# Optimization experiments

Measured on AMD Instinct MI355X. Metric: run time of the kernel, lower is better.

## Reference

```python
import jax, jax.numpy as jnp
import numpy as np

FIELD_DIMS = [1000000, 100000, 1008, 1004, 102, 1000, 500, 50, 112, 107]
B = 16384
EMB = 32
DENSE = 16
MLP = [256, 128, 64]
BN_EPS = 1e-5
V_TOTAL = int(np.sum(FIELD_DIMS))
OFFSETS = jnp.asarray(np.concatenate([[0], np.cumsum(FIELD_DIMS)[:-1]]), dtype=jnp.int64)


def _xavier(key, fan_out, fan_in):
    lim = float(np.sqrt(6.0 / (fan_in + fan_out)))
    return jax.random.uniform(key, (fan_out, fan_in), jnp.float32, -lim, lim)


def setup_inputs() -> dict:
    key = jax.random.key(0)
    ks = jax.random.split(key, 16)
    # per-field in-range indices, stacked to [B, n_fields]
    sparse_cols = [jax.random.randint(jax.random.fold_in(ks[0], i), (B,), 0, d)
                   for i, d in enumerate(FIELD_DIMS)]
    sparse_inputs = jnp.stack(sparse_cols, axis=1).astype(jnp.int64)
    dense_inputs = jax.random.normal(ks[1], (B, DENSE), jnp.float32)
    # concatenated embedding / first-order bias tables (same math as per-field nn.Embedding)
    emb_table = 0.01 * jax.random.normal(ks[2], (V_TOTAL, EMB), jnp.float32)
    bias_table = 0.01 * jax.random.normal(ks[3], (V_TOTAL, 1), jnp.float32)
    fm_bias = jnp.zeros((1,), jnp.float32)
    dims = [len(FIELD_DIMS) * EMB + DENSE] + MLP
    params = {}
    for li in range(len(MLP)):
        params[f"W{li}"] = _xavier(ks[4 + li], dims[li + 1], dims[li])
        params[f"b{li}"] = jnp.zeros((dims[li + 1],), jnp.float32)
        params[f"g{li}"] = jnp.ones((dims[li + 1],), jnp.float32)
        params[f"be{li}"] = jnp.zeros((dims[li + 1],), jnp.float32)
    Wo = _xavier(ks[10], 1, MLP[-1])
    bo = jnp.zeros((1,), jnp.float32)
    return dict(sparse_inputs=sparse_inputs, dense_inputs=dense_inputs,
                emb_table=emb_table, bias_table=bias_table, fm_bias=fm_bias,
                Wo=Wo, bo=bo, **params)


def reference(sparse_inputs, dense_inputs, emb_table, bias_table, fm_bias,
              Wo, bo, W0, b0, g0, be0, W1, b1, g1, be1, W2, b2, g2, be2):
    idx = sparse_inputs + OFFSETS[None, :]           # [B, F] global rows
    field_embs = emb_table[idx]                      # [B, F, E] multi-table gather
    # FM first order: sum of per-field scalar biases
    fm_first = bias_table[idx][..., 0].sum(axis=1)   # [B]
    # FM second order: 0.5 * sum_d ((sum_f e)^2 - sum_f e^2)
    s = field_embs.sum(axis=1)                       # [B, E]
    sq = (field_embs * field_embs).sum(axis=1)       # [B, E]
    fm_second = 0.5 * (s * s - sq).sum(axis=-1)      # [B]
    fm_out = fm_bias[0] + fm_first + fm_second
    # deep component (BatchNorm in eval mode at init stats: mean=0, var=1; dropout=identity)
    x = jnp.concatenate([field_embs.reshape(field_embs.shape[0], -1), dense_inputs], axis=-1)
    inv = 1.0 / jnp.sqrt(1.0 + BN_EPS)
    for W, b, g, be in ((W0, b0, g0, be0), (W1, b1, g1, be1), (W2, b2, g2, be2)):
        h = x @ W.T + b
        h = h * (g * inv) + be
        x = jax.nn.relu(h)
    deep_out = (x @ Wo.T + bo)[:, 0]
    return jax.nn.sigmoid(fm_out + deep_out)
```

## Files before the change

kernel.cpp:

```cpp
#include <hip/hip_runtime.h>
#include <hip/hip_bf16.h>
#include <math.h>

#define BROWS 16384
#define NF    10
#define EMB   32
#define DENSE 16
#define K0S   352
#define K0    336
#define N0    256
#define N1    128
#define N2    64
#define BN_INV 0.99999500003749969f

__constant__ int c_offsets[NF] = {
    0, 1000000, 1100000, 1101008, 1102012,
    1102114, 1103114, 1103614, 1103664, 1103776
};

typedef short  bf16x8 __attribute__((ext_vector_type(8)));
typedef float  f32x4  __attribute__((ext_vector_type(4)));

static __device__ __forceinline__ unsigned short f2bf(float x) {
    union { float f; unsigned u; } c; c.f = x;
    unsigned r = (c.u + 0x7FFFu + ((c.u >> 16) & 1u)) >> 16;
    return (unsigned short)r;
}

__global__ __launch_bounds__(256) void k_wconv_all(
    const float* __restrict__ W0, const float* __restrict__ W1,
    const float* __restrict__ W2,
    unsigned short* __restrict__ W0b, unsigned short* __restrict__ W1b,
    unsigned short* __restrict__ W2b)
{
    int i = blockIdx.x * 256 + threadIdx.x;
    if (i < N0 * K0S) {
        int r = i / K0S, c = i - r * K0S;
        W0b[i] = f2bf(c < K0 ? W0[r * K0 + c] : 0.f);
    } else if (i < N0 * K0S + N1 * N0) {
        int j = i - N0 * K0S;
        W1b[j] = f2bf(W1[j]);
    } else {
        int j = i - (N0 * K0S + N1 * N0);
        W2b[j] = f2bf(W2[j]);
    }
}

__global__ __launch_bounds__(256) void k_fused_l0(
    const int*   __restrict__ sparse,
    const float* __restrict__ dense,
    const float* __restrict__ emb,
    const float* __restrict__ bias_tab,
    const float* __restrict__ fm_bias,
    const unsigned short* __restrict__ W0b,
    const float* __restrict__ b0, const float* __restrict__ g0,
    const float* __restrict__ be0,
    unsigned short* __restrict__ x1,
    float* __restrict__ fm)
{
    const int tid  = threadIdx.x;
    const int wave = tid >> 6;
    const int lane = tid & 63;
    const int l16  = lane & 15;
    const int quad = lane >> 4;
    const int arow = blockIdx.x * 64 + wave * 16 + l16;

    int idx[NF];
#pragma unroll
    for (int f = 0; f < NF; ++f)
        idx[f] = sparse[arow * NF + f] + c_offsets[f];

    float first = 0.f;
    if (quad == 0) {
#pragma unroll
        for (int f = 0; f < NF; ++f) first += bias_tab[idx[f]];
    }

    float s8[8];
#pragma unroll
    for (int j = 0; j < 8; ++j) s8[j] = 0.f;
    float sq = 0.f;

    f32x4 acc[16];
#pragma unroll
    for (int nt = 0; nt < 16; ++nt) acc[nt] = (f32x4){0.f, 0.f, 0.f, 0.f};

#pragma unroll
    for (int f = 0; f < NF; ++f) {
        const float4* ep = (const float4*)(emb + (size_t)idx[f] * EMB + quad * 8);
        float4 v0 = ep[0];
        float4 v1 = ep[1];
        s8[0] += v0.x; s8[1] += v0.y; s8[2] += v0.z; s8[3] += v0.w;
        s8[4] += v1.x; s8[5] += v1.y; s8[6] += v1.z; s8[7] += v1.w;
        sq += v0.x*v0.x + v0.y*v0.y + v0.z*v0.z + v0.w*v0.w
            + v1.x*v1.x + v1.y*v1.y + v1.z*v1.z + v1.w*v1.w;
        bf16x8 a;
        a[0] = (short)f2bf(v0.x); a[1] = (short)f2bf(v0.y);
        a[2] = (short)f2bf(v0.z); a[3] = (short)f2bf(v0.w);
        a[4] = (short)f2bf(v1.x); a[5] = (short)f2bf(v1.y);
        a[6] = (short)f2bf(v1.z); a[7] = (short)f2bf(v1.w);
        const unsigned short* wp = W0b + (size_t)l16 * K0S + f * 32 + quad * 8;
#pragma unroll
        for (int nt = 0; nt < 16; ++nt) {
            bf16x8 w = *(const bf16x8*)(wp + (size_t)(nt * 16) * K0S);
            acc[nt] = __builtin_amdgcn_mfma_f32_16x16x32_bf16(a, w, acc[nt], 0, 0, 0);
        }
    }

    {
        bf16x8 a;
        if (quad < 2) {
            const float4* dp = (const float4*)(dense + arow * DENSE + quad * 8);
            float4 v0 = dp[0];
            float4 v1 = dp[1];
            a[0] = (short)f2bf(v0.x); a[1] = (short)f2bf(v0.y);
            a[2] = (short)f2bf(v0.z); a[3] = (short)f2bf(v0.w);
            a[4] = (short)f2bf(v1.x); a[5] = (short)f2bf(v1.y);
            a[6] = (short)f2bf(v1.z); a[7] = (short)f2bf(v1.w);
        } else {
#pragma unroll
            for (int j = 0; j < 8; ++j) a[j] = 0;
        }
        const unsigned short* wp = W0b + (size_t)l16 * K0S + 320 + quad * 8;
#pragma unroll
        for (int nt = 0; nt < 16; ++nt) {
            bf16x8 w = *(const bf16x8*)(wp + (size_t)(nt * 16) * K0S);
            acc[nt] = __builtin_amdgcn_mfma_f32_16x16x32_bf16(a, w, acc[nt], 0, 0, 0);
        }
    }

    float ss = 0.f;
#pragma unroll
    for (int j = 0; j < 8; ++j) ss += s8[j] * s8[j];
    ss += __shfl_xor(ss, 16); ss += __shfl_xor(ss, 32);
    sq += __shfl_xor(sq, 16); sq += __shfl_xor(sq, 32);
    first += __shfl_xor(first, 16); first += __shfl_xor(first, 32);
    if (quad == 0)
        fm[arow] = fm_bias[0] + first + 0.5f * (ss - sq);

#pragma unroll
    for (int nt = 0; nt < 16; ++nt) {
        int col = nt * 16 + l16;
        float sc = g0[col] * BN_INV;
        float tb = fmaf(b0[col], sc, be0[col]);
#pragma unroll
        for (int r = 0; r < 4; ++r) {
            int orow = blockIdx.x * 64 + wave * 16 + quad * 4 + r;
            float v = fmaf(acc[nt][r], sc, tb);
            v = v > 0.f ? v : 0.f;
            x1[(size_t)orow * N0 + col] = f2bf(v);
        }
    }
}

__global__ __launch_bounds__(256) void k_fused_tail(
    const unsigned short* __restrict__ x1,
    const unsigned short* __restrict__ W1b,
    const float* __restrict__ b1, const float* __restrict__ g1,
    const float* __restrict__ be1,
    const unsigned short* __restrict__ W2b,
    const float* __restrict__ b2, const float* __restrict__ g2,
    const float* __restrict__ be2,
    const float* __restrict__ Wo,
    const float* __restrict__ bo,
    const float* __restrict__ fm,
    float* __restrict__ out)
{
    __shared__ unsigned short h2[64][N1 + 8];

    const int tid  = threadIdx.x;
    const int wave = tid >> 6;
    const int lane = tid & 63;
    const int l16  = lane & 15;
    const int quad = lane >> 4;
    const int bm   = blockIdx.x * 64;
    const int arow = bm + wave * 16 + l16;

    f32x4 acc1[8];
#pragma unroll
    for (int nt = 0; nt < 8; ++nt) acc1[nt] = (f32x4){0.f, 0.f, 0.f, 0.f};
    const unsigned short* ap1 = x1 + (size_t)arow * N0 + quad * 8;
#pragma unroll
    for (int ks = 0; ks < 8; ++ks) {
        bf16x8 a = *(const bf16x8*)(ap1 + ks * 32);
        const unsigned short* wp = W1b + (size_t)l16 * N0 + ks * 32 + quad * 8;
#pragma unroll
        for (int nt = 0; nt < 8; ++nt) {
            bf16x8 w = *(const bf16x8*)(wp + (size_t)(nt * 16) * N0);
            acc1[nt] = __builtin_amdgcn_mfma_f32_16x16x32_bf16(a, w, acc1[nt], 0, 0, 0);
        }
    }
#pragma unroll
    for (int nt = 0; nt < 8; ++nt) {
        int col = nt * 16 + l16;
        float sc = g1[col] * BN_INV;
        float tb = fmaf(b1[col], sc, be1[col]);
#pragma unroll
        for (int r = 0; r < 4; ++r) {
            float v = fmaf(acc1[nt][r], sc, tb);
            v = v > 0.f ? v : 0.f;
            h2[wave * 16 + quad * 4 + r][col] = f2bf(v);
        }
    }
    __syncthreads();

    f32x4 acc2[4];
#pragma unroll
    for (int nt = 0; nt < 4; ++nt) acc2[nt] = (f32x4){0.f, 0.f, 0.f, 0.f};
#pragma unroll
    for (int ks = 0; ks < 4; ++ks) {
        bf16x8 a = *(const bf16x8*)(&h2[wave * 16 + l16][ks * 32 + quad * 8]);
        const unsigned short* wp = W2b + (size_t)l16 * N1 + ks * 32 + quad * 8;
#pragma unroll
        for (int nt = 0; nt < 4; ++nt) {
            bf16x8 w = *(const bf16x8*)(wp + (size_t)(nt * 16) * N1);
            acc2[nt] = __builtin_amdgcn_mfma_f32_16x16x32_bf16(a, w, acc2[nt], 0, 0, 0);
        }
    }

    float p[4] = {0.f, 0.f, 0.f, 0.f};
#pragma unroll
    for (int nt = 0; nt < 4; ++nt) {
        int col = nt * 16 + l16;
        float sc = g2[col] * BN_INV;
        float tb = fmaf(b2[col], sc, be2[col]);
        float wo = Wo[col];
#pragma unroll
        for (int r = 0; r < 4; ++r) {
            float v = fmaf(acc2[nt][r], sc, tb);
            v = v > 0.f ? v : 0.f;
            p[r] = fmaf(v, wo, p[r]);
        }
    }
#pragma unroll
    for (int r = 0; r < 4; ++r) {
        p[r] += __shfl_xor(p[r], 1);
        p[r] += __shfl_xor(p[r], 2);
        p[r] += __shfl_xor(p[r], 4);
        p[r] += __shfl_xor(p[r], 8);
    }
    if (l16 == 0) {
#pragma unroll
        for (int r = 0; r < 4; ++r) {
            int orow = bm + wave * 16 + quad * 4 + r;
            float z = fm[orow] + p[r] + bo[0];
            out[orow] = 1.f / (1.f + expf(-z));
        }
    }
}

extern "C" void kernel_launch(void* const* d_in, const int* in_sizes, int n_in,
                              void* d_out, int out_size, void* d_ws, size_t ws_size,
                              hipStream_t stream)
{
    const int*   sparse   = (const int*)  d_in[0];
    const float* dense    = (const float*)d_in[1];
    const float* emb      = (const float*)d_in[2];
    const float* bias_tab = (const float*)d_in[3];
    const float* fm_bias  = (const float*)d_in[4];
    const float* Wo       = (const float*)d_in[5];
    const float* bo       = (const float*)d_in[6];
    const float* W0 = (const float*)d_in[7];
    const float* b0 = (const float*)d_in[8];
    const float* g0 = (const float*)d_in[9];
    const float* be0= (const float*)d_in[10];
    const float* W1 = (const float*)d_in[11];
    const float* b1 = (const float*)d_in[12];
    const float* g1 = (const float*)d_in[13];
    const float* be1= (const float*)d_in[14];
    const float* W2 = (const float*)d_in[15];
    const float* b2 = (const float*)d_in[16];
    const float* g2 = (const float*)d_in[17];
    const float* be2= (const float*)d_in[18];

    float* out = (float*)d_out;

    char* p = (char*)d_ws;
    unsigned short* x1  = (unsigned short*)p; p += (size_t)BROWS * N0 * 2;
    unsigned short* W0b = (unsigned short*)p; p += (size_t)N0 * K0S * 2;
    unsigned short* W1b = (unsigned short*)p; p += (size_t)N1 * N0 * 2;
    unsigned short* W2b = (unsigned short*)p; p += (size_t)N2 * N1 * 2;
    float*          fm  = (float*)p;

    k_wconv_all<<<(N0 * K0S + N1 * N0 + N2 * N1) / 256, 256, 0, stream>>>(
        W0, W1, W2, W0b, W1b, W2b);

    k_fused_l0<<<BROWS / 64, 256, 0, stream>>>(
        sparse, dense, emb, bias_tab, fm_bias, W0b, b0, g0, be0, x1, fm);

    k_fused_tail<<<BROWS / 64, 256, 0, stream>>>(
        x1, W1b, b1, g1, be1, W2b, b2, g2, be2, Wo, bo, fm, out);
}
```

Before: 245.9 us.

## Fuse embedding layer and MLP tail into one kernel with LDS intermediates

```diff
diff --git a/kernel.cpp b/kernel.cpp
--- a/kernel.cpp
+++ b/kernel.cpp
@@ -46,7 +46,7 @@
     }
 }
 
-__global__ __launch_bounds__(256) void k_fused_l0(
+__global__ __launch_bounds__(256) void k_fused_all(
     const int*   __restrict__ sparse,
     const float* __restrict__ dense,
     const float* __restrict__ emb,
@@ -55,106 +55,6 @@
     const unsigned short* __restrict__ W0b,
     const float* __restrict__ b0, const float* __restrict__ g0,
     const float* __restrict__ be0,
-    unsigned short* __restrict__ x1,
-    float* __restrict__ fm)
-{
-    const int tid  = threadIdx.x;
-    const int wave = tid >> 6;
-    const int lane = tid & 63;
-    const int l16  = lane & 15;
-    const int quad = lane >> 4;
-    const int arow = blockIdx.x * 64 + wave * 16 + l16;
-
-    int idx[NF];
-#pragma unroll
-    for (int f = 0; f < NF; ++f)
-        idx[f] = sparse[arow * NF + f] + c_offsets[f];
-
-    float first = 0.f;
-    if (quad == 0) {
-#pragma unroll
-        for (int f = 0; f < NF; ++f) first += bias_tab[idx[f]];
-    }
-
-    float s8[8];
-#pragma unroll
-    for (int j = 0; j < 8; ++j) s8[j] = 0.f;
-    float sq = 0.f;
-
-    f32x4 acc[16];
-#pragma unroll
-    for (int nt = 0; nt < 16; ++nt) acc[nt] = (f32x4){0.f, 0.f, 0.f, 0.f};
-
-#pragma unroll
-    for (int f = 0; f < NF; ++f) {
-        const float4* ep = (const float4*)(emb + (size_t)idx[f] * EMB + quad * 8);
-        float4 v0 = ep[0];
-        float4 v1 = ep[1];
-        s8[0] += v0.x; s8[1] += v0.y; s8[2] += v0.z; s8[3] += v0.w;
-        s8[4] += v1.x; s8[5] += v1.y; s8[6] += v1.z; s8[7] += v1.w;
-        sq += v0.x*v0.x + v0.y*v0.y + v0.z*v0.z + v0.w*v0.w
-            + v1.x*v1.x + v1.y*v1.y + v1.z*v1.z + v1.w*v1.w;
-        bf16x8 a;
-        a[0] = (short)f2bf(v0.x); a[1] = (short)f2bf(v0.y);
-        a[2] = (short)f2bf(v0.z); a[3] = (short)f2bf(v0.w);
-        a[4] = (short)f2bf(v1.x); a[5] = (short)f2bf(v1.y);
-        a[6] = (short)f2bf(v1.z); a[7] = (short)f2bf(v1.w);
-        const unsigned short* wp = W0b + (size_t)l16 * K0S + f * 32 + quad * 8;
-#pragma unroll
-        for (int nt = 0; nt < 16; ++nt) {
-            bf16x8 w = *(const bf16x8*)(wp + (size_t)(nt * 16) * K0S);
-            acc[nt] = __builtin_amdgcn_mfma_f32_16x16x32_bf16(a, w, acc[nt], 0, 0, 0);
-        }
-    }
-
-    {
-        bf16x8 a;
-        if (quad < 2) {
-            const float4* dp = (const float4*)(dense + arow * DENSE + quad * 8);
-            float4 v0 = dp[0];
-            float4 v1 = dp[1];
-            a[0] = (short)f2bf(v0.x); a[1] = (short)f2bf(v0.y);
-            a[2] = (short)f2bf(v0.z); a[3] = (short)f2bf(v0.w);
-            a[4] = (short)f2bf(v1.x); a[5] = (short)f2bf(v1.y);
-            a[6] = (short)f2bf(v1.z); a[7] = (short)f2bf(v1.w);
-        } else {
-#pragma unroll
-            for (int j = 0; j < 8; ++j) a[j] = 0;
-        }
-        const unsigned short* wp = W0b + (size_t)l16 * K0S + 320 + quad * 8;
-#pragma unroll
-        for (int nt = 0; nt < 16; ++nt) {
-            bf16x8 w = *(const bf16x8*)(wp + (size_t)(nt * 16) * K0S);
-            acc[nt] = __builtin_amdgcn_mfma_f32_16x16x32_bf16(a, w, acc[nt], 0, 0, 0);
-        }
-    }
-
-    float ss = 0.f;
-#pragma unroll
-    for (int j = 0; j < 8; ++j) ss += s8[j] * s8[j];
-    ss += __shfl_xor(ss, 16); ss += __shfl_xor(ss, 32);
-    sq += __shfl_xor(sq, 16); sq += __shfl_xor(sq, 32);
-    first += __shfl_xor(first, 16); first += __shfl_xor(first, 32);
-    if (quad == 0)
-        fm[arow] = fm_bias[0] + first + 0.5f * (ss - sq);
-
-#pragma unroll
-    for (int nt = 0; nt < 16; ++nt) {
-        int col = nt * 16 + l16;
-        float sc = g0[col] * BN_INV;
-        float tb = fmaf(b0[col], sc, be0[col]);
-#pragma unroll
-        for (int r = 0; r < 4; ++r) {
-            int orow = blockIdx.x * 64 + wave * 16 + quad * 4 + r;
-            float v = fmaf(acc[nt][r], sc, tb);
-            v = v > 0.f ? v : 0.f;
-            x1[(size_t)orow * N0 + col] = f2bf(v);
-        }
-    }
-}
-
-__global__ __launch_bounds__(256) void k_fused_tail(
-    const unsigned short* __restrict__ x1,
     const unsigned short* __restrict__ W1b,
     const float* __restrict__ b1, const float* __restrict__ g1,
     const float* __restrict__ be1,
@@ -163,43 +63,108 @@
     const float* __restrict__ be2,
     const float* __restrict__ Wo,
     const float* __restrict__ bo,
-    const float* __restrict__ fm,
     float* __restrict__ out)
 {
-    __shared__ unsigned short h2[64][N1 + 8];
+    __shared__ unsigned short x1s[32][N0 + 2];
+    __shared__ unsigned short h2s[32][N1 + 2];
+    __shared__ float fmld[32];
+    __shared__ float partial[2][32];
 
     const int tid  = threadIdx.x;
     const int wave = tid >> 6;
     const int lane = tid & 63;
     const int l16  = lane & 15;
     const int quad = lane >> 4;
-    const int bm   = blockIdx.x * 64;
-    const int arow = bm + wave * 16 + l16;
+    const int rg   = wave & 1;
+    const int hh   = wave >> 1;
+    const int bm   = blockIdx.x * 32;
+    const int arow = bm + rg * 16 + l16;
+
+    int idx[NF];
+#pragma unroll
+    for (int f = 0; f < NF; ++f)
+        idx[f] = sparse[arow * NF + f] + c_offsets[f];
+
+    float first = 0.f, sq = 0.f;
+    float s8[8];
+#pragma unroll
+    for (int j = 0; j < 8; ++j) s8[j] = 0.f;
+
+    if (hh == 0 && quad == 0) {
+#pragma unroll
+        for (int f = 0; f < NF; ++f) first += bias_tab[idx[f]];
+    }
 
     f32x4 acc1[8];
 #pragma unroll
     for (int nt = 0; nt < 8; ++nt) acc1[nt] = (f32x4){0.f, 0.f, 0.f, 0.f};
-    const unsigned short* ap1 = x1 + (size_t)arow * N0 + quad * 8;
-#pragma unroll
-    for (int ks = 0; ks < 8; ++ks) {
-        bf16x8 a = *(const bf16x8*)(ap1 + ks * 32);
-        const unsigned short* wp = W1b + (size_t)l16 * N0 + ks * 32 + quad * 8;
+
+    const unsigned short* wp0 = W0b + (size_t)(hh * 128 + l16) * K0S + quad * 8;
+
+#pragma unroll
+    for (int f = 0; f < NF; ++f) {
+        const float4* ep = (const float4*)(emb + (size_t)idx[f] * EMB) + quad * 2;
+        float4 v0 = ep[0];
+        float4 v1 = ep[1];
+        if (hh == 0) {
+            s8[0] += v0.x; s8[1] += v0.y; s8[2] += v0.z; s8[3] += v0.w;
+            s8[4] += v1.x; s8[5] += v1.y; s8[6] += v1.z; s8[7] += v1.w;
+            sq += v0.x*v0.x + v0.y*v0.y + v0.z*v0.z + v0.w*v0.w
+                + v1.x*v1.x + v1.y*v1.y + v1.z*v1.z + v1.w*v1.w;
+        }
+        bf16x8 a;
+        a[0] = (short)f2bf(v0.x); a[1] = (short)f2bf(v0.y);
+        a[2] = (short)f2bf(v0.z); a[3] = (short)f2bf(v0.w);
+        a[4] = (short)f2bf(v1.x); a[5] = (short)f2bf(v1.y);
+        a[6] = (short)f2bf(v1.z); a[7] = (short)f2bf(v1.w);
 #pragma unroll
         for (int nt = 0; nt < 8; ++nt) {
-            bf16x8 w = *(const bf16x8*)(wp + (size_t)(nt * 16) * N0);
+            bf16x8 w = *(const bf16x8*)(wp0 + (size_t)(nt * 16) * K0S + f * 32);
             acc1[nt] = __builtin_amdgcn_mfma_f32_16x16x32_bf16(a, w, acc1[nt], 0, 0, 0);
         }
     }
+    {
+        bf16x8 a;
+        if (quad < 2) {
+            const float4* dp = (const float4*)(dense + arow * DENSE) + quad * 2;
+            float4 v0 = dp[0];
+            float4 v1 = dp[1];
+            a[0] = (short)f2bf(v0.x); a[1] = (short)f2bf(v0.y);
+            a[2] = (short)f2bf(v0.z); a[3] = (short)f2bf(v0.w);
+            a[4] = (short)f2bf(v1.x); a[5] = (short)f2bf(v1.y);
+            a[6] = (short)f2bf(v1.z); a[7] = (short)f2bf(v1.w);
+        } else {
+#pragma unroll
+            for (int j = 0; j < 8; ++j) a[j] = 0;
+        }
+#pragma unroll
+        for (int nt = 0; nt < 8; ++nt) {
+            bf16x8 w = *(const bf16x8*)(wp0 + (size_t)(nt * 16) * K0S + 320);
+            acc1[nt] = __builtin_amdgcn_mfma_f32_16x16x32_bf16(a, w, acc1[nt], 0, 0, 0);
+        }
+    }
+
+    if (hh == 0) {
+        float ss = 0.f;
+#pragma unroll
+        for (int j = 0; j < 8; ++j) ss += s8[j] * s8[j];
+        ss += __shfl_xor(ss, 16); ss += __shfl_xor(ss, 32);
+        sq += __shfl_xor(sq, 16); sq += __shfl_xor(sq, 32);
+        first += __shfl_xor(first, 16); first += __shfl_xor(first, 32);
+        if (quad == 0)
+            fmld[rg * 16 + l16] = fm_bias[0] + first + 0.5f * (ss - sq);
+    }
+
 #pragma unroll
     for (int nt = 0; nt < 8; ++nt) {
-        int col = nt * 16 + l16;
-        float sc = g1[col] * BN_INV;
-        float tb = fmaf(b1[col], sc, be1[col]);
+        int col = hh * 128 + nt * 16 + l16;
+        float sc = g0[col] * BN_INV;
+        float tb = fmaf(b0[col], sc, be0[col]);
 #pragma unroll
         for (int r = 0; r < 4; ++r) {
             float v = fmaf(acc1[nt][r], sc, tb);
             v = v > 0.f ? v : 0.f;
-            h2[wave * 16 + quad * 4 + r][col] = f2bf(v);
+            x1s[rg * 16 + quad * 4 + r][col] = f2bf(v);
         }
     }
     __syncthreads();
@@ -207,27 +172,54 @@
     f32x4 acc2[4];
 #pragma unroll
     for (int nt = 0; nt < 4; ++nt) acc2[nt] = (f32x4){0.f, 0.f, 0.f, 0.f};
+    const unsigned short* wp1 = W1b + (size_t)(hh * 64 + l16) * N0 + quad * 8;
+#pragma unroll
+    for (int ks = 0; ks < 8; ++ks) {
+        bf16x8 a = *(const bf16x8*)(&x1s[rg * 16 + l16][ks * 32 + quad * 8]);
+#pragma unroll
+        for (int nt = 0; nt < 4; ++nt) {
+            bf16x8 w = *(const bf16x8*)(wp1 + (size_t)(nt * 16) * N0 + ks * 32);
+            acc2[nt] = __builtin_amdgcn_mfma_f32_16x16x32_bf16(a, w, acc2[nt], 0, 0, 0);
+        }
+    }
+#pragma unroll
+    for (int nt = 0; nt < 4; ++nt) {
+        int col = hh * 64 + nt * 16 + l16;
+        float sc = g1[col] * BN_INV;
+        float tb = fmaf(b1[col], sc, be1[col]);
+#pragma unroll
+        for (int r = 0; r < 4; ++r) {
+            float v = fmaf(acc2[nt][r], sc, tb);
+            v = v > 0.f ? v : 0.f;
+            h2s[rg * 16 + quad * 4 + r][col] = f2bf(v);
+        }
+    }
+    __syncthreads();
+
+    f32x4 acc3[2];
+#pragma unroll
+    for (int nt = 0; nt < 2; ++nt) acc3[nt] = (f32x4){0.f, 0.f, 0.f, 0.f};
+    const unsigned short* wp2 = W2b + (size_t)(hh * 32 + l16) * N1 + quad * 8;
 #pragma unroll
     for (int ks = 0; ks < 4; ++ks) {
-        bf16x8 a = *(const bf16x8*)(&h2[wave * 16 + l16][ks * 32 + quad * 8]);
-        const unsigned short* wp = W2b + (size_t)l16 * N1 + ks * 32 + quad * 8;
-#pragma unroll
-        for (int nt = 0; nt < 4; ++nt) {
-            bf16x8 w = *(const bf16x8*)(wp + (size_t)(nt * 16) * N1);
-            acc2[nt] = __builtin_amdgcn_mfma_f32_16x16x32_bf16(a, w, acc2[nt], 0, 0, 0);
+        bf16x8 a = *(const bf16x8*)(&h2s[rg * 16 + l16][ks * 32 + quad * 8]);
+#pragma unroll
+        for (int nt = 0; nt < 2; ++nt) {
+            bf16x8 w = *(const bf16x8*)(wp2 + (size_t)(nt * 16) * N1 + ks * 32);
+            acc3[nt] = __builtin_amdgcn_mfma_f32_16x16x32_bf16(a, w, acc3[nt], 0, 0, 0);
         }
     }
 
     float p[4] = {0.f, 0.f, 0.f, 0.f};
 #pragma unroll
-    for (int nt = 0; nt < 4; ++nt) {
-        int col = nt * 16 + l16;
+    for (int nt = 0; nt < 2; ++nt) {
+        int col = hh * 32 + nt * 16 + l16;
         float sc = g2[col] * BN_INV;
         float tb = fmaf(b2[col], sc, be2[col]);
         float wo = Wo[col];
 #pragma unroll
         for (int r = 0; r < 4; ++r) {
-            float v = fmaf(acc2[nt][r], sc, tb);
+            float v = fmaf(acc3[nt][r], sc, tb);
             v = v > 0.f ? v : 0.f;
             p[r] = fmaf(v, wo, p[r]);
         }
@@ -241,11 +233,14 @@
     }
     if (l16 == 0) {
 #pragma unroll
-        for (int r = 0; r < 4; ++r) {
-            int orow = bm + wave * 16 + quad * 4 + r;
-            float z = fm[orow] + p[r] + bo[0];
-            out[orow] = 1.f / (1.f + expf(-z));
-        }
+        for (int r = 0; r < 4; ++r)
+            partial[hh][rg * 16 + quad * 4 + r] = p[r];
+    }
+    __syncthreads();
+
+    if (tid < 32) {
+        float z = fmld[tid] + partial[0][tid] + partial[1][tid] + bo[0];
+        out[bm + tid] = 1.f / (1.f + expf(-z));
     }
 }
 
@@ -276,18 +271,15 @@
     float* out = (float*)d_out;
 
     char* p = (char*)d_ws;
-    unsigned short* x1  = (unsigned short*)p; p += (size_t)BROWS * N0 * 2;
     unsigned short* W0b = (unsigned short*)p; p += (size_t)N0 * K0S * 2;
     unsigned short* W1b = (unsigned short*)p; p += (size_t)N1 * N0 * 2;
     unsigned short* W2b = (unsigned short*)p; p += (size_t)N2 * N1 * 2;
-    float*          fm  = (float*)p;
 
     k_wconv_all<<<(N0 * K0S + N1 * N0 + N2 * N1) / 256, 256, 0, stream>>>(
         W0, W1, W2, W0b, W1b, W2b);
 
-    k_fused_l0<<<BROWS / 64, 256, 0, stream>>>(
-        sparse, dense, emb, bias_tab, fm_bias, W0b, b0, g0, be0, x1, fm);
-
-    k_fused_tail<<<BROWS / 64, 256, 0, stream>>>(
-        x1, W1b, b1, g1, be1, W2b, b2, g2, be2, Wo, bo, fm, out);
-}
+    k_fused_all<<<BROWS / 32, 256, 0, stream>>>(
+        sparse, dense, emb, bias_tab, fm_bias,
+        W0b, b0, g0, be0, W1b, b1, g1, be1, W2b, b2, g2, be2,
+        Wo, bo, out);
+}
```

After: 235.7 us. 4.1% less time.
